# Optimization experiments

Measured on AMD Instinct MI355X. Metric: run time of the kernel, lower is better.

Reference implementation:

```python
import jax, jax.numpy as jnp
import numpy as np

DIM = 64
N_EMBED = 2048
BETA = 0.25
B, H, W = 16, 64, 64


def setup_inputs() -> dict:
    key = jax.random.key(0)
    k1, k2 = jax.random.split(key)
    inp = jax.random.normal(k1, (B, DIM, H, W), dtype=jnp.float32)
    r = 1.0 / N_EMBED
    embeddings = jax.random.uniform(k2, (DIM, N_EMBED), minval=-r, maxval=r, dtype=jnp.float32)
    return {"input": inp, "embeddings": embeddings}


def reference(input, embeddings):
    sg = jax.lax.stop_gradient
    # (B,C,H,W) -> (B,H,W,C) -> (B*H*W, C)
    x = jnp.transpose(input, (0, 2, 3, 1))
    flat = x.reshape(-1, x.shape[-1])
    # squared L2 distances to each codebook vector: (N, n_embed)
    dist = (flat * flat).sum(1, keepdims=True) - 2.0 * (flat @ embeddings) \
        + (embeddings * embeddings).sum(0, keepdims=True)
    embed_ind = jnp.argmin(dist, axis=1).reshape(x.shape[:-1])  # (B,H,W)
    # gather codes: embeddings.T is (n_embed, dim); result (B,H,W,C) -> (B,C,H,W)
    quantize = jnp.transpose(embeddings.T[embed_ind], (0, 3, 1, 2))
    loss = jnp.mean((sg(quantize) - input) ** 2) \
        + BETA * jnp.mean((quantize - sg(input)) ** 2)
    # straight-through estimator
    quantize_st = input + sg(quantize - input)
    return quantize_st, loss, embed_ind
```

## Files before the change

### kernel.cpp

```cpp
#include <hip/hip_runtime.h>


#define HW     4096
#define CHW    262144
#define NE     2048
#define OUT_Q  4194304
#define WS_SE  0
#define WS_ACC 2048
#define INF    3.402823466e38f

__global__ __launch_bounds__(256) void vq_prep(const float* __restrict__ emb,
                                               float* __restrict__ ws) {
  int j = blockIdx.x * 256 + threadIdx.x;
  float s = 0.0f;
  for (int k = 0; k < 64; ++k) {
    float e = emb[k * NE + j];
    s = __fadd_rn(s, __fmul_rn(e, e));
  }
  ws[WS_SE + j] = s;
  if (j == 0) ws[WS_ACC] = 0.0f;
}

#define SQ(v) __fmul_rn(v, v)
#define UPD(i, A, J) { \
  float dist = __fadd_rn(__fsub_rn(sx##i, __fmul_rn(2.0f, A)), sej); \
  if (dist < best##i) { best##i = dist; bi##i = cj + J; } }

__global__ __launch_bounds__(256) void vq_main(const float* __restrict__ inp,
                                               const float* __restrict__ emb,
                                               const float* __restrict__ se,
                                               float* __restrict__ out,
                                               float* __restrict__ loss_acc) {
  __shared__ __align__(16) float xs[64][64];
  __shared__ __align__(16) float es[64][64];
  __shared__ __align__(16) float sxs[64];
  __shared__ float rvv[16][64];
  __shared__ int   rii[16][64];
  __shared__ int   bixs[64];
  __shared__ float lss[4];

  const int tx   = threadIdx.x;
  const int b    = blockIdx.x >> 6;
  const int hw0  = (blockIdx.x & 63) * 64;
  const int pixbase = blockIdx.x * 64;
  const float* xg = inp + (size_t)b * CHW + hw0;

  {
    int pix = tx & 63, kr = tx >> 6;
#pragma unroll
    for (int pass = 0; pass < 16; ++pass) {
      int k = pass * 4 + kr;
      xs[k][pix] = xg[k * HW + pix];
    }
  }
  __syncthreads();

  if (tx < 64) {
    int p = tx;
    float r0 = SQ(xs[0][p]), r1 = SQ(xs[1][p]), r2 = SQ(xs[2][p]), r3 = SQ(xs[3][p]);
    float r4 = SQ(xs[4][p]), r5 = SQ(xs[5][p]), r6 = SQ(xs[6][p]), r7 = SQ(xs[7][p]);
#pragma unroll
    for (int blk = 1; blk < 8; ++blk) {
      r0 = __fadd_rn(r0, SQ(xs[blk * 8 + 0][p]));
      r1 = __fadd_rn(r1, SQ(xs[blk * 8 + 1][p]));
      r2 = __fadd_rn(r2, SQ(xs[blk * 8 + 2][p]));
      r3 = __fadd_rn(r3, SQ(xs[blk * 8 + 3][p]));
      r4 = __fadd_rn(r4, SQ(xs[blk * 8 + 4][p]));
      r5 = __fadd_rn(r5, SQ(xs[blk * 8 + 5][p]));
      r6 = __fadd_rn(r6, SQ(xs[blk * 8 + 6][p]));
      r7 = __fadd_rn(r7, SQ(xs[blk * 8 + 7][p]));
    }
    sxs[p] = __fadd_rn(__fadd_rn(__fadd_rn(r0, r1), __fadd_rn(r2, r3)),
                       __fadd_rn(__fadd_rn(r4, r5), __fadd_rn(r6, r7)));
  }
  __syncthreads();

  const int pg = tx & 15, cg = tx >> 4;
  const float4 sxv = *reinterpret_cast<const float4*>(&sxs[pg * 4]);
  const float sx0 = sxv.x, sx1 = sxv.y, sx2 = sxv.z, sx3 = sxv.w;

  float best0 = INF, best1 = INF, best2 = INF, best3 = INF;
  int   bi0 = 0, bi1 = 0, bi2 = 0, bi3 = 0;

  const float4* xr = reinterpret_cast<const float4*>(&xs[0][0]);
  const float4* er = reinterpret_cast<const float4*>(&es[0][0]);
  const int ecc = tx & 63, ekr = tx >> 6;

#pragma unroll 1
  for (int ch = 0; ch < 32; ++ch) {
    const int cbase = ch * 64;
    const float4 sev = *reinterpret_cast<const float4*>(&se[cbase + cg * 4]);

#pragma unroll
    for (int pass = 0; pass < 16; ++pass) {
      int k = pass * 4 + ekr;
      es[k][ecc] = emb[k * NE + cbase + ecc];
    }
    __syncthreads();

    float a00 = 0.f, a01 = 0.f, a02 = 0.f, a03 = 0.f;
    float a10 = 0.f, a11 = 0.f, a12 = 0.f, a13 = 0.f;
    float a20 = 0.f, a21 = 0.f, a22 = 0.f, a23 = 0.f;
    float a30 = 0.f, a31 = 0.f, a32 = 0.f, a33 = 0.f;
#pragma unroll 8
    for (int k = 0; k < 64; ++k) {
      float4 av = xr[k * 16 + pg];
      float4 bv = er[k * 16 + cg];
      a00 = __fmaf_rn(av.x, bv.x, a00); a01 = __fmaf_rn(av.x, bv.y, a01);
      a02 = __fmaf_rn(av.x, bv.z, a02); a03 = __fmaf_rn(av.x, bv.w, a03);
      a10 = __fmaf_rn(av.y, bv.x, a10); a11 = __fmaf_rn(av.y, bv.y, a11);
      a12 = __fmaf_rn(av.y, bv.z, a12); a13 = __fmaf_rn(av.y, bv.w, a13);
      a20 = __fmaf_rn(av.z, bv.x, a20); a21 = __fmaf_rn(av.z, bv.y, a21);
      a22 = __fmaf_rn(av.z, bv.z, a22); a23 = __fmaf_rn(av.z, bv.w, a23);
      a30 = __fmaf_rn(av.w, bv.x, a30); a31 = __fmaf_rn(av.w, bv.y, a31);
      a32 = __fmaf_rn(av.w, bv.z, a32); a33 = __fmaf_rn(av.w, bv.w, a33);
    }

    const int cj = cbase + cg * 4;
    { const float sej = sev.x; UPD(0, a00, 0) UPD(1, a10, 0) UPD(2, a20, 0) UPD(3, a30, 0) }
    { const float sej = sev.y; UPD(0, a01, 1) UPD(1, a11, 1) UPD(2, a21, 1) UPD(3, a31, 1) }
    { const float sej = sev.z; UPD(0, a02, 2) UPD(1, a12, 2) UPD(2, a22, 2) UPD(3, a32, 2) }
    { const float sej = sev.w; UPD(0, a03, 3) UPD(1, a13, 3) UPD(2, a23, 3) UPD(3, a33, 3) }

    __syncthreads();
  }

  rvv[cg][pg * 4 + 0] = best0; rii[cg][pg * 4 + 0] = bi0;
  rvv[cg][pg * 4 + 1] = best1; rii[cg][pg * 4 + 1] = bi1;
  rvv[cg][pg * 4 + 2] = best2; rii[cg][pg * 4 + 2] = bi2;
  rvv[cg][pg * 4 + 3] = best3; rii[cg][pg * 4 + 3] = bi3;
  __syncthreads();
  if (tx < 64) {
    float bv = rvv[0][tx];
    int   bx = rii[0][tx];
#pragma unroll
    for (int g = 1; g < 16; ++g) {
      float v = rvv[g][tx];
      int   ix = rii[g][tx];
      if (v < bv || (v == bv && ix < bx)) { bv = v; bx = ix; }
    }
    bixs[tx] = bx;
    out[OUT_Q + 1 + pixbase + tx] = (float)bx;
  }
  __syncthreads();

  {
    int pix = tx & 63, grp = tx >> 6;
    int bx = bixs[pix];
    float* op = out + (size_t)b * CHW + hw0 + pix;
    float lsum = 0.0f;
#pragma unroll
    for (int ci = 0; ci < 16; ++ci) {
      int c = grp * 16 + ci;
      float xv = xs[c][pix];
      float qv = emb[(size_t)c * NE + bx];
      float d  = __fsub_rn(qv, xv);
      op[c * HW] = __fadd_rn(xv, d);
      lsum = __fadd_rn(lsum, __fmul_rn(d, d));
    }
#pragma unroll
    for (int off = 32; off > 0; off >>= 1)
      lsum = __fadd_rn(lsum, __shfl_xor(lsum, off, 64));
    if ((tx & 63) == 0) lss[tx >> 6] = lsum;
  }
  __syncthreads();
  if (tx == 0) {
    float s = __fadd_rn(__fadd_rn(lss[0], lss[1]), __fadd_rn(lss[2], lss[3]));
    atomicAdd(loss_acc, s);
  }
}

__global__ void vq_final(const float* __restrict__ ws, float* __restrict__ out) {
  float m = ws[WS_ACC] / 4194304.0f;
  out[OUT_Q] = __fadd_rn(m, __fmul_rn(0.25f, m));
}

extern "C" void kernel_launch(void* const* d_in, const int* in_sizes, int n_in,
                              void* d_out, int out_size, void* d_ws, size_t ws_size,
                              hipStream_t stream) {
  const float* inp = (const float*)d_in[0];
  const float* emb = (const float*)d_in[1];
  float* out = (float*)d_out;
  float* ws  = (float*)d_ws;

  vq_prep<<<8, 256, 0, stream>>>(emb, ws);
  vq_main<<<1024, 256, 0, stream>>>(inp, emb, ws + WS_SE, out, ws + WS_ACC);
  vq_final<<<1, 1, 0, stream>>>(ws, out);
}
```

Baseline: 311.4 us.

## Double-buffer codebook tiles with register prefetch and float4 global loads

Codebook chunks now go through two shared-memory buffers. The next chunk is loaded into registers at the start of each iteration and written to the alternate buffer after the compute, so global load latency overlaps the FMA loop and one barrier per iteration is removed. Input and embedding loads are also widened to float4. The cost is an extra 16KB of LDS and 16 more live registers, which may reduce occupancy.

```diff
diff --git a/kernel.cpp b/kernel.cpp
--- a/kernel.cpp
+++ b/kernel.cpp
@@ -32,7 +32,7 @@
                                                float* __restrict__ out,
                                                float* __restrict__ loss_acc) {
   __shared__ __align__(16) float xs[64][64];
-  __shared__ __align__(16) float es[64][64];
+  __shared__ __align__(16) float es[2][64][64];
   __shared__ __align__(16) float sxs[64];
   __shared__ float rvv[16][64];
   __shared__ int   rii[16][64];
@@ -43,16 +43,22 @@
   const int b    = blockIdx.x >> 6;
   const int hw0  = (blockIdx.x & 63) * 64;
   const int pixbase = blockIdx.x * 64;
-  const float* xg = inp + (size_t)b * CHW + hw0;
-
-  {
-    int pix = tx & 63, kr = tx >> 6;
-#pragma unroll
-    for (int pass = 0; pass < 16; ++pass) {
-      int k = pass * 4 + kr;
-      xs[k][pix] = xg[k * HW + pix];
-    }
-  }
+
+  const int r = tx >> 4, c = tx & 15;
+  const float4* eg4 = reinterpret_cast<const float4*>(emb);
+  const float4* xg4 = reinterpret_cast<const float4*>(inp + (size_t)b * CHW + hw0);
+  float4* xs4 = reinterpret_cast<float4*>(&xs[0][0]);
+
+#pragma unroll
+  for (int p = 0; p < 4; ++p)
+    xs4[(p * 16 + r) * 16 + c] = xg4[(size_t)(p * 16 + r) * 1024 + c];
+
+  const int eb0 = r * 512 + c;
+  float4 s0 = eg4[eb0];
+  float4 s1 = eg4[eb0 + 8192];
+  float4 s2 = eg4[eb0 + 16384];
+  float4 s3 = eg4[eb0 + 24576];
+
   __syncthreads();
 
   if (tx < 64) {
@@ -73,6 +79,14 @@
     sxs[p] = __fadd_rn(__fadd_rn(__fadd_rn(r0, r1), __fadd_rn(r2, r3)),
                        __fadd_rn(__fadd_rn(r4, r5), __fadd_rn(r6, r7)));
   }
+
+  {
+    float4* ew = reinterpret_cast<float4*>(&es[0][0][0]);
+    ew[r * 16 + c]       = s0;
+    ew[256 + r * 16 + c] = s1;
+    ew[512 + r * 16 + c] = s2;
+    ew[768 + r * 16 + c] = s3;
+  }
   __syncthreads();
 
   const int pg = tx & 15, cg = tx >> 4;
@@ -83,20 +97,20 @@
   int   bi0 = 0, bi1 = 0, bi2 = 0, bi3 = 0;
 
   const float4* xr = reinterpret_cast<const float4*>(&xs[0][0]);
-  const float4* er = reinterpret_cast<const float4*>(&es[0][0]);
-  const int ecc = tx & 63, ekr = tx >> 6;
 
 #pragma unroll 1
   for (int ch = 0; ch < 32; ++ch) {
+    if (ch < 31) {
+      const int nb = eb0 + (ch + 1) * 16;
+      s0 = eg4[nb];
+      s1 = eg4[nb + 8192];
+      s2 = eg4[nb + 16384];
+      s3 = eg4[nb + 24576];
+    }
     const int cbase = ch * 64;
     const float4 sev = *reinterpret_cast<const float4*>(&se[cbase + cg * 4]);
 
-#pragma unroll
-    for (int pass = 0; pass < 16; ++pass) {
-      int k = pass * 4 + ekr;
-      es[k][ecc] = emb[k * NE + cbase + ecc];
-    }
-    __syncthreads();
+    const float4* er = reinterpret_cast<const float4*>(&es[ch & 1][0][0]);
 
     float a00 = 0.f, a01 = 0.f, a02 = 0.f, a03 = 0.f;
     float a10 = 0.f, a11 = 0.f, a12 = 0.f, a13 = 0.f;
@@ -122,6 +136,13 @@
     { const float sej = sev.z; UPD(0, a02, 2) UPD(1, a12, 2) UPD(2, a22, 2) UPD(3, a32, 2) }
     { const float sej = sev.w; UPD(0, a03, 3) UPD(1, a13, 3) UPD(2, a23, 3) UPD(3, a33, 3) }
 
+    if (ch < 31) {
+      float4* ew = reinterpret_cast<float4*>(&es[(ch + 1) & 1][0][0]);
+      ew[r * 16 + c]       = s0;
+      ew[256 + r * 16 + c] = s1;
+      ew[512 + r * 16 + c] = s2;
+      ew[768 + r * 16 + c] = s3;
+    }
     __syncthreads();
   }
 
@@ -151,11 +172,11 @@
     float lsum = 0.0f;
 #pragma unroll
     for (int ci = 0; ci < 16; ++ci) {
-      int c = grp * 16 + ci;
-      float xv = xs[c][pix];
-      float qv = emb[(size_t)c * NE + bx];
+      int cch = grp * 16 + ci;
+      float xv = xs[cch][pix];
+      float qv = emb[(size_t)cch * NE + bx];
       float d  = __fsub_rn(qv, xv);
-      op[c * HW] = __fadd_rn(xv, d);
+      op[cch * HW] = __fadd_rn(xv, d);
       lsum = __fadd_rn(lsum, __fmul_rn(d, d));
     }
 #pragma unroll
```

After: 302.7 us. -2.8%, faster.

## Enlarge VQ tile to 128x128 with register-prefetched codebook and 8x8 microtile

Applied to the files above, without the earlier changes.

Each block now handles 128 pixels against 128-code chunks, and each thread computes an 8x8 register microtile instead of 4x4. This raises FMA-to-LDS-load intensity and halves the grid. The next codebook chunk is loaded into registers with float4 global loads while the current chunk is computed, then stored to shared memory, so global latency overlaps compute. Shared layout uses a swizzled float4 index to avoid bank conflicts. The cost is higher register pressure, which may lower occupancy, and fewer blocks (512) on the device.

```diff
diff --git a/kernel.cpp b/kernel.cpp
--- a/kernel.cpp
+++ b/kernel.cpp
@@ -21,122 +21,188 @@
   if (j == 0) ws[WS_ACC] = 0.0f;
 }
 
-#define SQ(v) __fmul_rn(v, v)
-#define UPD(i, A, J) { \
-  float dist = __fadd_rn(__fsub_rn(sx##i, __fmul_rn(2.0f, A)), sej); \
-  if (dist < best##i) { best##i = dist; bi##i = cj + J; } }
+#define F4ZERO(v) { v.x = 0.f; v.y = 0.f; v.z = 0.f; v.w = 0.f; }
+#define F4ADD(d, a, b) { d.x = __fadd_rn(a.x, b.x); d.y = __fadd_rn(a.y, b.y); \
+                         d.z = __fadd_rn(a.z, b.z); d.w = __fadd_rn(a.w, b.w); }
+#define F4SQACC(r, v) { r.x = __fadd_rn(r.x, __fmul_rn(v.x, v.x)); \
+                        r.y = __fadd_rn(r.y, __fmul_rn(v.y, v.y)); \
+                        r.z = __fadd_rn(r.z, __fmul_rn(v.z, v.z)); \
+                        r.w = __fadd_rn(r.w, __fmul_rn(v.w, v.w)); }
+#define FMA8(p, a) { \
+  C##p##a_.x = __fmaf_rn(a, bv0.x, C##p##a_.x); C##p##a_.y = __fmaf_rn(a, bv0.y, C##p##a_.y); \
+  C##p##a_.z = __fmaf_rn(a, bv0.z, C##p##a_.z); C##p##a_.w = __fmaf_rn(a, bv0.w, C##p##a_.w); \
+  C##p##b_.x = __fmaf_rn(a, bv1.x, C##p##b_.x); C##p##b_.y = __fmaf_rn(a, bv1.y, C##p##b_.y); \
+  C##p##b_.z = __fmaf_rn(a, bv1.z, C##p##b_.z); C##p##b_.w = __fmaf_rn(a, bv1.w, C##p##b_.w); }
+#define DECLC(p) float4 C##p##a_, C##p##b_;
+#define ZEROC(p) { F4ZERO(C##p##a_) F4ZERO(C##p##b_) }
+#define UPD1(p, q, comp, J) { \
+  float dd = __fadd_rn(__fsub_rn(sx_##p, __fmul_rn(2.0f, C##p##q.comp)), sej); \
+  if (dd < bb##p) { bb##p = dd; ii##p = jj + (J); } }
+#define UPD8(q, comp, J, SE) { const float sej = (SE); \
+  UPD1(0,q,comp,J) UPD1(1,q,comp,J) UPD1(2,q,comp,J) UPD1(3,q,comp,J) \
+  UPD1(4,q,comp,J) UPD1(5,q,comp,J) UPD1(6,q,comp,J) UPD1(7,q,comp,J) }
 
 __global__ __launch_bounds__(256) void vq_main(const float* __restrict__ inp,
                                                const float* __restrict__ emb,
                                                const float* __restrict__ se,
                                                float* __restrict__ out,
                                                float* __restrict__ loss_acc) {
-  __shared__ __align__(16) float xs[64][64];
-  __shared__ __align__(16) float es[64][64];
-  __shared__ __align__(16) float sxs[64];
-  __shared__ float rvv[16][64];
-  __shared__ int   rii[16][64];
-  __shared__ int   bixs[64];
-  __shared__ float lss[4];
+  __shared__ __align__(16) float xsw[8192];
+  __shared__ __align__(16) float esw[8192];
+  float4* xsw4 = reinterpret_cast<float4*>(xsw);
+  float4* esw4 = reinterpret_cast<float4*>(esw);
+  float* rvv  = esw;
+  int*   rii  = reinterpret_cast<int*>(esw + 2048);
+  int*   bixs = reinterpret_cast<int*>(esw + 4096);
+  float* lss  = esw + 4224;
 
   const int tx   = threadIdx.x;
-  const int b    = blockIdx.x >> 6;
-  const int hw0  = (blockIdx.x & 63) * 64;
-  const int pixbase = blockIdx.x * 64;
-  const float* xg = inp + (size_t)b * CHW + hw0;
-
+  const int b    = blockIdx.x >> 5;
+  const int hw0  = (blockIdx.x & 31) << 7;
+  const int pixbase = blockIdx.x << 7;
+
+  const int rr = tx >> 5, qc = tx & 31;
+  const int qp = ((qc & 1) << 4) | (qc >> 1);
+  const float4* xg4 = reinterpret_cast<const float4*>(inp + (size_t)b * CHW);
+  const float4* eg4 = reinterpret_cast<const float4*>(emb);
+  const float4* se4 = reinterpret_cast<const float4*>(se);
+  const int hwq = hw0 >> 2;
+
+  float4 xl0 = xg4[(0*8 + rr) * 1024 + hwq + qc];
+  float4 xl1 = xg4[(1*8 + rr) * 1024 + hwq + qc];
+  float4 xl2 = xg4[(2*8 + rr) * 1024 + hwq + qc];
+  float4 xl3 = xg4[(3*8 + rr) * 1024 + hwq + qc];
+  float4 xl4 = xg4[(4*8 + rr) * 1024 + hwq + qc];
+  float4 xl5 = xg4[(5*8 + rr) * 1024 + hwq + qc];
+  float4 xl6 = xg4[(6*8 + rr) * 1024 + hwq + qc];
+  float4 xl7 = xg4[(7*8 + rr) * 1024 + hwq + qc];
+  float4 st0 = eg4[(0*8 + rr) * 512 + qc];
+  float4 st1 = eg4[(1*8 + rr) * 512 + qc];
+  float4 st2 = eg4[(2*8 + rr) * 512 + qc];
+  float4 st3 = eg4[(3*8 + rr) * 512 + qc];
+  float4 st4 = eg4[(4*8 + rr) * 512 + qc];
+  float4 st5 = eg4[(5*8 + rr) * 512 + qc];
+  float4 st6 = eg4[(6*8 + rr) * 512 + qc];
+  float4 st7 = eg4[(7*8 + rr) * 512 + qc];
+  xsw4[(0*8 + rr) * 32 + qp] = xl0;  xsw4[(1*8 + rr) * 32 + qp] = xl1;
+  xsw4[(2*8 + rr) * 32 + qp] = xl2;  xsw4[(3*8 + rr) * 32 + qp] = xl3;
+  xsw4[(4*8 + rr) * 32 + qp] = xl4;  xsw4[(5*8 + rr) * 32 + qp] = xl5;
+  xsw4[(6*8 + rr) * 32 + qp] = xl6;  xsw4[(7*8 + rr) * 32 + qp] = xl7;
+  esw4[(0*8 + rr) * 32 + qp] = st0;  esw4[(1*8 + rr) * 32 + qp] = st1;
+  esw4[(2*8 + rr) * 32 + qp] = st2;  esw4[(3*8 + rr) * 32 + qp] = st3;
+  esw4[(4*8 + rr) * 32 + qp] = st4;  esw4[(5*8 + rr) * 32 + qp] = st5;
+  esw4[(6*8 + rr) * 32 + qp] = st6;  esw4[(7*8 + rr) * 32 + qp] = st7;
+  __syncthreads();
+
+  const int pg = tx & 15, cg = tx >> 4;
+
+  float sx_0, sx_1, sx_2, sx_3, sx_4, sx_5, sx_6, sx_7;
   {
-    int pix = tx & 63, kr = tx >> 6;
-#pragma unroll
-    for (int pass = 0; pass < 16; ++pass) {
-      int k = pass * 4 + kr;
-      xs[k][pix] = xg[k * HW + pix];
-    }
-  }
-  __syncthreads();
-
-  if (tx < 64) {
-    int p = tx;
-    float r0 = SQ(xs[0][p]), r1 = SQ(xs[1][p]), r2 = SQ(xs[2][p]), r3 = SQ(xs[3][p]);
-    float r4 = SQ(xs[4][p]), r5 = SQ(xs[5][p]), r6 = SQ(xs[6][p]), r7 = SQ(xs[7][p]);
-#pragma unroll
-    for (int blk = 1; blk < 8; ++blk) {
-      r0 = __fadd_rn(r0, SQ(xs[blk * 8 + 0][p]));
-      r1 = __fadd_rn(r1, SQ(xs[blk * 8 + 1][p]));
-      r2 = __fadd_rn(r2, SQ(xs[blk * 8 + 2][p]));
-      r3 = __fadd_rn(r3, SQ(xs[blk * 8 + 3][p]));
-      r4 = __fadd_rn(r4, SQ(xs[blk * 8 + 4][p]));
-      r5 = __fadd_rn(r5, SQ(xs[blk * 8 + 5][p]));
-      r6 = __fadd_rn(r6, SQ(xs[blk * 8 + 6][p]));
-      r7 = __fadd_rn(r7, SQ(xs[blk * 8 + 7][p]));
-    }
-    sxs[p] = __fadd_rn(__fadd_rn(__fadd_rn(r0, r1), __fadd_rn(r2, r3)),
-                       __fadd_rn(__fadd_rn(r4, r5), __fadd_rn(r6, r7)));
-  }
-  __syncthreads();
-
-  const int pg = tx & 15, cg = tx >> 4;
-  const float4 sxv = *reinterpret_cast<const float4*>(&sxs[pg * 4]);
-  const float sx0 = sxv.x, sx1 = sxv.y, sx2 = sxv.z, sx3 = sxv.w;
-
-  float best0 = INF, best1 = INF, best2 = INF, best3 = INF;
-  int   bi0 = 0, bi1 = 0, bi2 = 0, bi3 = 0;
-
-  const float4* xr = reinterpret_cast<const float4*>(&xs[0][0]);
-  const float4* er = reinterpret_cast<const float4*>(&es[0][0]);
-  const int ecc = tx & 63, ekr = tx >> 6;
+    float4 r0, r1, r2, r3, r4, r5, r6, r7;
+    F4ZERO(r0) F4ZERO(r1) F4ZERO(r2) F4ZERO(r3)
+    F4ZERO(r4) F4ZERO(r5) F4ZERO(r6) F4ZERO(r7)
+#pragma unroll
+    for (int blk = 0; blk < 8; ++blk) {
+      float4 v;
+      v = xsw4[(blk*8 + 0) * 32 + pg]; F4SQACC(r0, v)
+      v = xsw4[(blk*8 + 1) * 32 + pg]; F4SQACC(r1, v)
+      v = xsw4[(blk*8 + 2) * 32 + pg]; F4SQACC(r2, v)
+      v = xsw4[(blk*8 + 3) * 32 + pg]; F4SQACC(r3, v)
+      v = xsw4[(blk*8 + 4) * 32 + pg]; F4SQACC(r4, v)
+      v = xsw4[(blk*8 + 5) * 32 + pg]; F4SQACC(r5, v)
+      v = xsw4[(blk*8 + 6) * 32 + pg]; F4SQACC(r6, v)
+      v = xsw4[(blk*8 + 7) * 32 + pg]; F4SQACC(r7, v)
+    }
+    float4 t01, t23, t45, t67, ta, tb, sq;
+    F4ADD(t01, r0, r1) F4ADD(t23, r2, r3) F4ADD(t45, r4, r5) F4ADD(t67, r6, r7)
+    F4ADD(ta, t01, t23) F4ADD(tb, t45, t67) F4ADD(sq, ta, tb)
+    sx_0 = sq.x; sx_1 = sq.y; sx_2 = sq.z; sx_3 = sq.w;
+  }
+  {
+    float4 r0, r1, r2, r3, r4, r5, r6, r7;
+    F4ZERO(r0) F4ZERO(r1) F4ZERO(r2) F4ZERO(r3)
+    F4ZERO(r4) F4ZERO(r5) F4ZERO(r6) F4ZERO(r7)
+#pragma unroll
+    for (int blk = 0; blk < 8; ++blk) {
+      float4 v;
+      v = xsw4[(blk*8 + 0) * 32 + 16 + pg]; F4SQACC(r0, v)
+      v = xsw4[(blk*8 + 1) * 32 + 16 + pg]; F4SQACC(r1, v)
+      v = xsw4[(blk*8 + 2) * 32 + 16 + pg]; F4SQACC(r2, v)
+      v = xsw4[(blk*8 + 3) * 32 + 16 + pg]; F4SQACC(r3, v)
+      v = xsw4[(blk*8 + 4) * 32 + 16 + pg]; F4SQACC(r4, v)
+      v = xsw4[(blk*8 + 5) * 32 + 16 + pg]; F4SQACC(r5, v)
+      v = xsw4[(blk*8 + 6) * 32 + 16 + pg]; F4SQACC(r6, v)
+      v = xsw4[(blk*8 + 7) * 32 + 16 + pg]; F4SQACC(r7, v)
+    }
+    float4 t01, t23, t45, t67, ta, tb, sq;
+    F4ADD(t01, r0, r1) F4ADD(t23, r2, r3) F4ADD(t45, r4, r5) F4ADD(t67, r6, r7)
+    F4ADD(ta, t01, t23) F4ADD(tb, t45, t67) F4ADD(sq, ta, tb)
+    sx_4 = sq.x; sx_5 = sq.y; sx_6 = sq.z; sx_7 = sq.w;
+  }
+
+  float bb0 = INF, bb1 = INF, bb2 = INF, bb3 = INF;
+  float bb4 = INF, bb5 = INF, bb6 = INF, bb7 = INF;
+  int   ii0 = 0, ii1 = 0, ii2 = 0, ii3 = 0, ii4 = 0, ii5 = 0, ii6 = 0, ii7 = 0;
 
 #pragma unroll 1
-  for (int ch = 0; ch < 32; ++ch) {
-    const int cbase = ch * 64;
-    const float4 sev = *reinterpret_cast<const float4*>(&se[cbase + cg * 4]);
-
-#pragma unroll
-    for (int pass = 0; pass < 16; ++pass) {
-      int k = pass * 4 + ekr;
-      es[k][ecc] = emb[k * NE + cbase + ecc];
-    }
-    __syncthreads();
-
-    float a00 = 0.f, a01 = 0.f, a02 = 0.f, a03 = 0.f;
-    float a10 = 0.f, a11 = 0.f, a12 = 0.f, a13 = 0.f;
-    float a20 = 0.f, a21 = 0.f, a22 = 0.f, a23 = 0.f;
-    float a30 = 0.f, a31 = 0.f, a32 = 0.f, a33 = 0.f;
+  for (int ch = 0; ch < 16; ++ch) {
+    if (ch < 15) {
+      const int cb = (ch + 1) * 32;
+      st0 = eg4[(0*8 + rr) * 512 + cb + qc];
+      st1 = eg4[(1*8 + rr) * 512 + cb + qc];
+      st2 = eg4[(2*8 + rr) * 512 + cb + qc];
+      st3 = eg4[(3*8 + rr) * 512 + cb + qc];
+      st4 = eg4[(4*8 + rr) * 512 + cb + qc];
+      st5 = eg4[(5*8 + rr) * 512 + cb + qc];
+      st6 = eg4[(6*8 + rr) * 512 + cb + qc];
+      st7 = eg4[(7*8 + rr) * 512 + cb + qc];
+    }
+    const float4 sea = se4[ch * 32 + cg * 2];
+    const float4 seb = se4[ch * 32 + cg * 2 + 1];
+
+    DECLC(0) DECLC(1) DECLC(2) DECLC(3) DECLC(4) DECLC(5) DECLC(6) DECLC(7)
+    ZEROC(0) ZEROC(1) ZEROC(2) ZEROC(3) ZEROC(4) ZEROC(5) ZEROC(6) ZEROC(7)
+
 #pragma unroll 8
     for (int k = 0; k < 64; ++k) {
-      float4 av = xr[k * 16 + pg];
-      float4 bv = er[k * 16 + cg];
-      a00 = __fmaf_rn(av.x, bv.x, a00); a01 = __fmaf_rn(av.x, bv.y, a01);
-      a02 = __fmaf_rn(av.x, bv.z, a02); a03 = __fmaf_rn(av.x, bv.w, a03);
-      a10 = __fmaf_rn(av.y, bv.x, a10); a11 = __fmaf_rn(av.y, bv.y, a11);
-      a12 = __fmaf_rn(av.y, bv.z, a12); a13 = __fmaf_rn(av.y, bv.w, a13);
-      a20 = __fmaf_rn(av.z, bv.x, a20); a21 = __fmaf_rn(av.z, bv.y, a21);
-      a22 = __fmaf_rn(av.z, bv.z, a22); a23 = __fmaf_rn(av.z, bv.w, a23);
-      a30 = __fmaf_rn(av.w, bv.x, a30); a31 = __fmaf_rn(av.w, bv.y, a31);
-      a32 = __fmaf_rn(av.w, bv.z, a32); a33 = __fmaf_rn(av.w, bv.w, a33);
-    }
-
-    const int cj = cbase + cg * 4;
-    { const float sej = sev.x; UPD(0, a00, 0) UPD(1, a10, 0) UPD(2, a20, 0) UPD(3, a30, 0) }
-    { const float sej = sev.y; UPD(0, a01, 1) UPD(1, a11, 1) UPD(2, a21, 1) UPD(3, a31, 1) }
-    { const float sej = sev.z; UPD(0, a02, 2) UPD(1, a12, 2) UPD(2, a22, 2) UPD(3, a32, 2) }
-    { const float sej = sev.w; UPD(0, a03, 3) UPD(1, a13, 3) UPD(2, a23, 3) UPD(3, a33, 3) }
+      const float4 av0 = xsw4[k * 32 + pg];
+      const float4 av1 = xsw4[k * 32 + 16 + pg];
+      const float4 bv0 = esw4[k * 32 + cg];
+      const float4 bv1 = esw4[k * 32 + 16 + cg];
+      FMA8(0, av0.x) FMA8(1, av0.y) FMA8(2, av0.z) FMA8(3, av0.w)
+      FMA8(4, av1.x) FMA8(5, av1.y) FMA8(6, av1.z) FMA8(7, av1.w)
+    }
+
+    const int jj = ch * 128 + cg * 8;
+    UPD8(a_, x, 0, sea.x) UPD8(a_, y, 1, sea.y) UPD8(a_, z, 2, sea.z) UPD8(a_, w, 3, sea.w)
+    UPD8(b_, x, 4, seb.x) UPD8(b_, y, 5, seb.y) UPD8(b_, z, 6, seb.z) UPD8(b_, w, 7, seb.w)
 
     __syncthreads();
-  }
-
-  rvv[cg][pg * 4 + 0] = best0; rii[cg][pg * 4 + 0] = bi0;
-  rvv[cg][pg * 4 + 1] = best1; rii[cg][pg * 4 + 1] = bi1;
-  rvv[cg][pg * 4 + 2] = best2; rii[cg][pg * 4 + 2] = bi2;
-  rvv[cg][pg * 4 + 3] = best3; rii[cg][pg * 4 + 3] = bi3;
-  __syncthreads();
-  if (tx < 64) {
-    float bv = rvv[0][tx];
-    int   bx = rii[0][tx];
+    if (ch < 15) {
+      esw4[(0*8 + rr) * 32 + qp] = st0;  esw4[(1*8 + rr) * 32 + qp] = st1;
+      esw4[(2*8 + rr) * 32 + qp] = st2;  esw4[(3*8 + rr) * 32 + qp] = st3;
+      esw4[(4*8 + rr) * 32 + qp] = st4;  esw4[(5*8 + rr) * 32 + qp] = st5;
+      esw4[(6*8 + rr) * 32 + qp] = st6;  esw4[(7*8 + rr) * 32 + qp] = st7;
+    }
+    __syncthreads();
+  }
+
+  rvv[cg * 128 + pg * 8 + 0] = bb0;  rii[cg * 128 + pg * 8 + 0] = ii0;
+  rvv[cg * 128 + pg * 8 + 1] = bb1;  rii[cg * 128 + pg * 8 + 1] = ii1;
+  rvv[cg * 128 + pg * 8 + 2] = bb2;  rii[cg * 128 + pg * 8 + 2] = ii2;
+  rvv[cg * 128 + pg * 8 + 3] = bb3;  rii[cg * 128 + pg * 8 + 3] = ii3;
+  rvv[cg * 128 + pg * 8 + 4] = bb4;  rii[cg * 128 + pg * 8 + 4] = ii4;
+  rvv[cg * 128 + pg * 8 + 5] = bb5;  rii[cg * 128 + pg * 8 + 5] = ii5;
+  rvv[cg * 128 + pg * 8 + 6] = bb6;  rii[cg * 128 + pg * 8 + 6] = ii6;
+  rvv[cg * 128 + pg * 8 + 7] = bb7;  rii[cg * 128 + pg * 8 + 7] = ii7;
+  __syncthreads();
+  if (tx < 128) {
+    float bv = rvv[tx];
+    int   bx = rii[tx];
 #pragma unroll
     for (int g = 1; g < 16; ++g) {
-      float v = rvv[g][tx];
-      int   ix = rii[g][tx];
+      float v  = rvv[g * 128 + tx];
+      int   ix = rii[g * 128 + tx];
       if (v < bv || (v == bv && ix < bx)) { bv = v; bx = ix; }
     }
     bixs[tx] = bx;
@@ -145,14 +211,16 @@
   __syncthreads();
 
   {
-    int pix = tx & 63, grp = tx >> 6;
-    int bx = bixs[pix];
+    const int pix = tx & 127, half = tx >> 7;
+    const int qx = pix >> 2, cmp = pix & 3;
+    const int qpix = (((qx & 1) << 4) | (qx >> 1)) * 4 + cmp;
+    const int bx = bixs[pix];
     float* op = out + (size_t)b * CHW + hw0 + pix;
     float lsum = 0.0f;
 #pragma unroll
-    for (int ci = 0; ci < 16; ++ci) {
-      int c = grp * 16 + ci;
-      float xv = xs[c][pix];
+    for (int ci = 0; ci < 32; ++ci) {
+      const int c = half * 32 + ci;
+      float xv = xsw[c * 128 + qpix];
       float qv = emb[(size_t)c * NE + bx];
       float d  = __fsub_rn(qv, xv);
       op[c * HW] = __fadd_rn(xv, d);
@@ -184,6 +252,6 @@
   float* ws  = (float*)d_ws;
 
   vq_prep<<<8, 256, 0, stream>>>(emb, ws);
-  vq_main<<<1024, 256, 0, stream>>>(inp, emb, ws + WS_SE, out, ws + WS_ACC);
+  vq_main<<<512, 256, 0, stream>>>(inp, emb, ws + WS_SE, out, ws + WS_ACC);
   vq_final<<<1, 1, 0, stream>>>(ws, out);
 }
```

Result: faster. 272.3 us (-12.6%).

## Enlarge VQ block tile to 256 pixels with double-buffered direct-to-LDS codebook loads

Applied to the files above, without the earlier changes.

Each block now handles 256 pixels against 128-code chunks, and each thread holds a 16x8 register tile instead of 4x4. This raises arithmetic intensity per LDS read. Codebook chunks are double-buffered in shared memory using global_load_lds, so the next chunk's fetch overlaps the current chunk's FMAs, and the reduction scratch reuses the codebook buffer. The costs are much higher register pressure, larger LDS use and lower occupancy. The grid also shrinks to 256 blocks, which is about one block per CU and may leave the machine underfilled.

```diff
diff --git a/kernel.cpp b/kernel.cpp
--- a/kernel.cpp
+++ b/kernel.cpp
@@ -21,122 +21,158 @@
   if (j == 0) ws[WS_ACC] = 0.0f;
 }
 
-#define SQ(v) __fmul_rn(v, v)
-#define UPD(i, A, J) { \
-  float dist = __fadd_rn(__fsub_rn(sx##i, __fmul_rn(2.0f, A)), sej); \
-  if (dist < best##i) { best##i = dist; bi##i = cj + J; } }
+__device__ __forceinline__ void gll16(const void* g, void* l) {
+  __builtin_amdgcn_global_load_lds(
+      (const __attribute__((address_space(1))) void*)g,
+      (__attribute__((address_space(3))) void*)l, 16, 0, 0);
+}
+
+#define F4ZERO(v) { v.x = 0.f; v.y = 0.f; v.z = 0.f; v.w = 0.f; }
+#define F4ADD(d, a, b) { d.x = __fadd_rn(a.x, b.x); d.y = __fadd_rn(a.y, b.y); \
+                         d.z = __fadd_rn(a.z, b.z); d.w = __fadd_rn(a.w, b.w); }
+#define F4SQACC(r, v) { r.x = __fadd_rn(r.x, __fmul_rn(v.x, v.x)); \
+                        r.y = __fadd_rn(r.y, __fmul_rn(v.y, v.y)); \
+                        r.z = __fadd_rn(r.z, __fmul_rn(v.z, v.z)); \
+                        r.w = __fadd_rn(r.w, __fmul_rn(v.w, v.w)); }
+#define FMA8(p, a) { \
+  C##p##a_.x = __fmaf_rn(a, bv0.x, C##p##a_.x); C##p##a_.y = __fmaf_rn(a, bv0.y, C##p##a_.y); \
+  C##p##a_.z = __fmaf_rn(a, bv0.z, C##p##a_.z); C##p##a_.w = __fmaf_rn(a, bv0.w, C##p##a_.w); \
+  C##p##b_.x = __fmaf_rn(a, bv1.x, C##p##b_.x); C##p##b_.y = __fmaf_rn(a, bv1.y, C##p##b_.y); \
+  C##p##b_.z = __fmaf_rn(a, bv1.z, C##p##b_.z); C##p##b_.w = __fmaf_rn(a, bv1.w, C##p##b_.w); }
+#define DECLC(p) float4 C##p##a_, C##p##b_;
+#define ZEROC(p) { F4ZERO(C##p##a_) F4ZERO(C##p##b_) }
+#define UPD1(p, q, comp, J) { \
+  float dd = __fadd_rn(__fsub_rn(sx_##p, __fmul_rn(2.0f, C##p##q.comp)), sej); \
+  if (dd < bb##p) { bb##p = dd; ii##p = jj + (J); } }
+#define UPD16(q, comp, J, SE) { const float sej = (SE); \
+  UPD1(0,q,comp,J)  UPD1(1,q,comp,J)  UPD1(2,q,comp,J)  UPD1(3,q,comp,J) \
+  UPD1(4,q,comp,J)  UPD1(5,q,comp,J)  UPD1(6,q,comp,J)  UPD1(7,q,comp,J) \
+  UPD1(8,q,comp,J)  UPD1(9,q,comp,J)  UPD1(10,q,comp,J) UPD1(11,q,comp,J) \
+  UPD1(12,q,comp,J) UPD1(13,q,comp,J) UPD1(14,q,comp,J) UPD1(15,q,comp,J) }
+#define STOR1(p) { const int px_ = ((p)>>2)*64 + pg*4 + ((p)&3); \
+  rvv[cg*256 + px_] = bb##p; rii[cg*256 + px_] = ii##p; }
+#define SXPASS(i, o0, o1, o2, o3) { \
+  float4 r0, r1, r2, r3, r4, r5, r6, r7; \
+  F4ZERO(r0) F4ZERO(r1) F4ZERO(r2) F4ZERO(r3) \
+  F4ZERO(r4) F4ZERO(r5) F4ZERO(r6) F4ZERO(r7) \
+  _Pragma("unroll") \
+  for (int blk = 0; blk < 8; ++blk) { \
+    float4 v; \
+    v = xs4[(blk*8 + 0) * 64 + (i)*16 + pg]; F4SQACC(r0, v) \
+    v = xs4[(blk*8 + 1) * 64 + (i)*16 + pg]; F4SQACC(r1, v) \
+    v = xs4[(blk*8 + 2) * 64 + (i)*16 + pg]; F4SQACC(r2, v) \
+    v = xs4[(blk*8 + 3) * 64 + (i)*16 + pg]; F4SQACC(r3, v) \
+    v = xs4[(blk*8 + 4) * 64 + (i)*16 + pg]; F4SQACC(r4, v) \
+    v = xs4[(blk*8 + 5) * 64 + (i)*16 + pg]; F4SQACC(r5, v) \
+    v = xs4[(blk*8 + 6) * 64 + (i)*16 + pg]; F4SQACC(r6, v) \
+    v = xs4[(blk*8 + 7) * 64 + (i)*16 + pg]; F4SQACC(r7, v) \
+  } \
+  float4 t01, t23, t45, t67, ta, tb, sq; \
+  F4ADD(t01, r0, r1) F4ADD(t23, r2, r3) F4ADD(t45, r4, r5) F4ADD(t67, r6, r7) \
+  F4ADD(ta, t01, t23) F4ADD(tb, t45, t67) F4ADD(sq, ta, tb) \
+  o0 = sq.x; o1 = sq.y; o2 = sq.z; o3 = sq.w; }
 
 __global__ __launch_bounds__(256) void vq_main(const float* __restrict__ inp,
                                                const float* __restrict__ emb,
                                                const float* __restrict__ se,
                                                float* __restrict__ out,
                                                float* __restrict__ loss_acc) {
-  __shared__ __align__(16) float xs[64][64];
-  __shared__ __align__(16) float es[64][64];
-  __shared__ __align__(16) float sxs[64];
-  __shared__ float rvv[16][64];
-  __shared__ int   rii[16][64];
-  __shared__ int   bixs[64];
-  __shared__ float lss[4];
+  __shared__ __align__(16) float xs[64 * 256];
+  __shared__ __align__(16) float es[2][64 * 128];
+  float* esf = &es[0][0];
+  const float4* xs4 = reinterpret_cast<const float4*>(xs);
+  float* rvv  = esf;
+  int*   rii  = reinterpret_cast<int*>(esf + 4096);
+  int*   bixs = reinterpret_cast<int*>(esf + 8192);
+  float* lss  = esf + 8448;
 
   const int tx   = threadIdx.x;
-  const int b    = blockIdx.x >> 6;
-  const int hw0  = (blockIdx.x & 63) * 64;
-  const int pixbase = blockIdx.x * 64;
-  const float* xg = inp + (size_t)b * CHW + hw0;
+  const int wv   = tx >> 6;
+  const int b    = blockIdx.x >> 4;
+  const int hw0  = (blockIdx.x & 15) << 8;
+  const int pixbase = blockIdx.x << 8;
 
   {
-    int pix = tx & 63, kr = tx >> 6;
-#pragma unroll
-    for (int pass = 0; pass < 16; ++pass) {
-      int k = pass * 4 + kr;
-      xs[k][pix] = xg[k * HW + pix];
-    }
-  }
-  __syncthreads();
-
-  if (tx < 64) {
-    int p = tx;
-    float r0 = SQ(xs[0][p]), r1 = SQ(xs[1][p]), r2 = SQ(xs[2][p]), r3 = SQ(xs[3][p]);
-    float r4 = SQ(xs[4][p]), r5 = SQ(xs[5][p]), r6 = SQ(xs[6][p]), r7 = SQ(xs[7][p]);
-#pragma unroll
-    for (int blk = 1; blk < 8; ++blk) {
-      r0 = __fadd_rn(r0, SQ(xs[blk * 8 + 0][p]));
-      r1 = __fadd_rn(r1, SQ(xs[blk * 8 + 1][p]));
-      r2 = __fadd_rn(r2, SQ(xs[blk * 8 + 2][p]));
-      r3 = __fadd_rn(r3, SQ(xs[blk * 8 + 3][p]));
-      r4 = __fadd_rn(r4, SQ(xs[blk * 8 + 4][p]));
-      r5 = __fadd_rn(r5, SQ(xs[blk * 8 + 5][p]));
-      r6 = __fadd_rn(r6, SQ(xs[blk * 8 + 6][p]));
-      r7 = __fadd_rn(r7, SQ(xs[blk * 8 + 7][p]));
-    }
-    sxs[p] = __fadd_rn(__fadd_rn(__fadd_rn(r0, r1), __fadd_rn(r2, r3)),
-                       __fadd_rn(__fadd_rn(r4, r5), __fadd_rn(r6, r7)));
+    const float* xsrc = inp + (size_t)b * CHW + hw0 + (tx & 63) * 4;
+#pragma unroll
+    for (int p = 0; p < 16; ++p)
+      gll16(xsrc + (p * 4 + wv) * HW, xs + (p * 4 + wv) * 256);
+    const float* esrc = emb + (size_t)(tx >> 5) * NE + (tx & 31) * 4;
+#pragma unroll
+    for (int p = 0; p < 8; ++p)
+      gll16(esrc + (p * 8) * NE, &es[0][0] + (p * 8 + 2 * wv) * 128);
   }
   __syncthreads();
 
   const int pg = tx & 15, cg = tx >> 4;
-  const float4 sxv = *reinterpret_cast<const float4*>(&sxs[pg * 4]);
-  const float sx0 = sxv.x, sx1 = sxv.y, sx2 = sxv.z, sx3 = sxv.w;
-
-  float best0 = INF, best1 = INF, best2 = INF, best3 = INF;
-  int   bi0 = 0, bi1 = 0, bi2 = 0, bi3 = 0;
-
-  const float4* xr = reinterpret_cast<const float4*>(&xs[0][0]);
-  const float4* er = reinterpret_cast<const float4*>(&es[0][0]);
-  const int ecc = tx & 63, ekr = tx >> 6;
+  const float4* se4 = reinterpret_cast<const float4*>(se);
+
+  float sx_0, sx_1, sx_2, sx_3, sx_4, sx_5, sx_6, sx_7;
+  float sx_8, sx_9, sx_10, sx_11, sx_12, sx_13, sx_14, sx_15;
+  SXPASS(0, sx_0, sx_1, sx_2, sx_3)
+  SXPASS(1, sx_4, sx_5, sx_6, sx_7)
+  SXPASS(2, sx_8, sx_9, sx_10, sx_11)
+  SXPASS(3, sx_12, sx_13, sx_14, sx_15)
+
+  float bb0 = INF, bb1 = INF, bb2 = INF, bb3 = INF;
+  float bb4 = INF, bb5 = INF, bb6 = INF, bb7 = INF;
+  float bb8 = INF, bb9 = INF, bb10 = INF, bb11 = INF;
+  float bb12 = INF, bb13 = INF, bb14 = INF, bb15 = INF;
+  int ii0 = 0, ii1 = 0, ii2 = 0, ii3 = 0, ii4 = 0, ii5 = 0, ii6 = 0, ii7 = 0;
+  int ii8 = 0, ii9 = 0, ii10 = 0, ii11 = 0, ii12 = 0, ii13 = 0, ii14 = 0, ii15 = 0;
+
+  const float* esrc = emb + (size_t)(tx >> 5) * NE + (tx & 31) * 4;
 
 #pragma unroll 1
-  for (int ch = 0; ch < 32; ++ch) {
-    const int cbase = ch * 64;
-    const float4 sev = *reinterpret_cast<const float4*>(&se[cbase + cg * 4]);
-
-#pragma unroll
-    for (int pass = 0; pass < 16; ++pass) {
-      int k = pass * 4 + ekr;
-      es[k][ecc] = emb[k * NE + cbase + ecc];
-    }
+  for (int ch = 0; ch < 16; ++ch) {
+    if (ch < 15) {
+      float* dst = &es[(ch + 1) & 1][0] + (2 * wv) * 128;
+      const float* src = esrc + (ch + 1) * 128;
+#pragma unroll
+      for (int p = 0; p < 8; ++p)
+        gll16(src + (p * 8) * NE, dst + (p * 8) * 128);
+    }
+    const float4 sea = se4[ch * 32 + cg * 2];
+    const float4 seb = se4[ch * 32 + cg * 2 + 1];
+
+    const float4* er4 = reinterpret_cast<const float4*>(&es[ch & 1][0]);
+
+    DECLC(0)  DECLC(1)  DECLC(2)  DECLC(3)  DECLC(4)  DECLC(5)  DECLC(6)  DECLC(7)
+    DECLC(8)  DECLC(9)  DECLC(10) DECLC(11) DECLC(12) DECLC(13) DECLC(14) DECLC(15)
+    ZEROC(0)  ZEROC(1)  ZEROC(2)  ZEROC(3)  ZEROC(4)  ZEROC(5)  ZEROC(6)  ZEROC(7)
+    ZEROC(8)  ZEROC(9)  ZEROC(10) ZEROC(11) ZEROC(12) ZEROC(13) ZEROC(14) ZEROC(15)
+
+#pragma unroll 2
+    for (int k = 0; k < 64; ++k) {
+      const float4 av0 = xs4[k * 64 + pg];
+      const float4 av1 = xs4[k * 64 + 16 + pg];
+      const float4 av2 = xs4[k * 64 + 32 + pg];
+      const float4 av3 = xs4[k * 64 + 48 + pg];
+      const float4 bv0 = er4[k * 32 + cg * 2];
+      const float4 bv1 = er4[k * 32 + cg * 2 + 1];
+      FMA8(0,  av0.x) FMA8(1,  av0.y) FMA8(2,  av0.z) FMA8(3,  av0.w)
+      FMA8(4,  av1.x) FMA8(5,  av1.y) FMA8(6,  av1.z) FMA8(7,  av1.w)
+      FMA8(8,  av2.x) FMA8(9,  av2.y) FMA8(10, av2.z) FMA8(11, av2.w)
+      FMA8(12, av3.x) FMA8(13, av3.y) FMA8(14, av3.z) FMA8(15, av3.w)
+    }
+
+    const int jj = ch * 128 + cg * 8;
+    UPD16(a_, x, 0, sea.x) UPD16(a_, y, 1, sea.y) UPD16(a_, z, 2, sea.z) UPD16(a_, w, 3, sea.w)
+    UPD16(b_, x, 4, seb.x) UPD16(b_, y, 5, seb.y) UPD16(b_, z, 6, seb.z) UPD16(b_, w, 7, seb.w)
+
     __syncthreads();
-
-    float a00 = 0.f, a01 = 0.f, a02 = 0.f, a03 = 0.f;
-    float a10 = 0.f, a11 = 0.f, a12 = 0.f, a13 = 0.f;
-    float a20 = 0.f, a21 = 0.f, a22 = 0.f, a23 = 0.f;
-    float a30 = 0.f, a31 = 0.f, a32 = 0.f, a33 = 0.f;
-#pragma unroll 8
-    for (int k = 0; k < 64; ++k) {
-      float4 av = xr[k * 16 + pg];
-      float4 bv = er[k * 16 + cg];
-      a00 = __fmaf_rn(av.x, bv.x, a00); a01 = __fmaf_rn(av.x, bv.y, a01);
-      a02 = __fmaf_rn(av.x, bv.z, a02); a03 = __fmaf_rn(av.x, bv.w, a03);
-      a10 = __fmaf_rn(av.y, bv.x, a10); a11 = __fmaf_rn(av.y, bv.y, a11);
-      a12 = __fmaf_rn(av.y, bv.z, a12); a13 = __fmaf_rn(av.y, bv.w, a13);
-      a20 = __fmaf_rn(av.z, bv.x, a20); a21 = __fmaf_rn(av.z, bv.y, a21);
-      a22 = __fmaf_rn(av.z, bv.z, a22); a23 = __fmaf_rn(av.z, bv.w, a23);
-      a30 = __fmaf_rn(av.w, bv.x, a30); a31 = __fmaf_rn(av.w, bv.y, a31);
-      a32 = __fmaf_rn(av.w, bv.z, a32); a33 = __fmaf_rn(av.w, bv.w, a33);
-    }
-
-    const int cj = cbase + cg * 4;
-    { const float sej = sev.x; UPD(0, a00, 0) UPD(1, a10, 0) UPD(2, a20, 0) UPD(3, a30, 0) }
-    { const float sej = sev.y; UPD(0, a01, 1) UPD(1, a11, 1) UPD(2, a21, 1) UPD(3, a31, 1) }
-    { const float sej = sev.z; UPD(0, a02, 2) UPD(1, a12, 2) UPD(2, a22, 2) UPD(3, a32, 2) }
-    { const float sej = sev.w; UPD(0, a03, 3) UPD(1, a13, 3) UPD(2, a23, 3) UPD(3, a33, 3) }
-
-    __syncthreads();
-  }
-
-  rvv[cg][pg * 4 + 0] = best0; rii[cg][pg * 4 + 0] = bi0;
-  rvv[cg][pg * 4 + 1] = best1; rii[cg][pg * 4 + 1] = bi1;
-  rvv[cg][pg * 4 + 2] = best2; rii[cg][pg * 4 + 2] = bi2;
-  rvv[cg][pg * 4 + 3] = best3; rii[cg][pg * 4 + 3] = bi3;
-  __syncthreads();
-  if (tx < 64) {
-    float bv = rvv[0][tx];
-    int   bx = rii[0][tx];
+  }
+
+  STOR1(0)  STOR1(1)  STOR1(2)  STOR1(3)  STOR1(4)  STOR1(5)  STOR1(6)  STOR1(7)
+  STOR1(8)  STOR1(9)  STOR1(10) STOR1(11) STOR1(12) STOR1(13) STOR1(14) STOR1(15)
+  __syncthreads();
+  {
+    float bv = rvv[tx];
+    int   bx = rii[tx];
 #pragma unroll
     for (int g = 1; g < 16; ++g) {
-      float v = rvv[g][tx];
-      int   ix = rii[g][tx];
+      float v  = rvv[g * 256 + tx];
+      int   ix = rii[g * 256 + tx];
       if (v < bv || (v == bv && ix < bx)) { bv = v; bx = ix; }
     }
     bixs[tx] = bx;
@@ -145,14 +181,12 @@
   __syncthreads();
 
   {
-    int pix = tx & 63, grp = tx >> 6;
-    int bx = bixs[pix];
-    float* op = out + (size_t)b * CHW + hw0 + pix;
+    const int bx = bixs[tx];
+    float* op = out + (size_t)b * CHW + hw0 + tx;
     float lsum = 0.0f;
-#pragma unroll
-    for (int ci = 0; ci < 16; ++ci) {
-      int c = grp * 16 + ci;
-      float xv = xs[c][pix];
+#pragma unroll 8
+    for (int c = 0; c < 64; ++c) {
+      float xv = xs[c * 256 + tx];
       float qv = emb[(size_t)c * NE + bx];
       float d  = __fsub_rn(qv, xv);
       op[c * HW] = __fadd_rn(xv, d);
@@ -161,7 +195,7 @@
 #pragma unroll
     for (int off = 32; off > 0; off >>= 1)
       lsum = __fadd_rn(lsum, __shfl_xor(lsum, off, 64));
-    if ((tx & 63) == 0) lss[tx >> 6] = lsum;
+    if ((tx & 63) == 0) lss[wv] = lsum;
   }
   __syncthreads();
   if (tx == 0) {
@@ -184,6 +218,6 @@
   float* ws  = (float*)d_ws;
 
   vq_prep<<<8, 256, 0, stream>>>(emb, ws);
-  vq_main<<<1024, 256, 0, stream>>>(inp, emb, ws + WS_SE, out, ws + WS_ACC);
+  vq_main<<<256, 256, 0, stream>>>(inp, emb, ws + WS_SE, out, ws + WS_ACC);
   vq_final<<<1, 1, 0, stream>>>(ws, out);
 }
```

Measured after the change: 282.0 us. 9.4% less time.
